# Kernel tuning notes

Hardware: AMD Instinct MI355X
Metric: run time of the kernel (lower is better)

## Reference

```python
import jax, jax.numpy as jnp
import numpy as np

D_MODEL = 512
BINS = 64


def setup_inputs() -> dict:
    key = jax.random.key(0)
    ks = jax.random.split(key, 5)
    x = jax.random.normal(ks[0], (1, 512, D_MODEL), dtype=jnp.float32)
    # torch Linear(2d, d): weight [d, 2d]; store transposed [2d, d] for x @ W
    s1 = 1.0 / np.sqrt(2 * D_MODEL)
    W1 = jax.random.uniform(ks[1], (2 * D_MODEL, D_MODEL), jnp.float32, -s1, s1)
    b1 = jax.random.uniform(ks[2], (D_MODEL,), jnp.float32, -s1, s1)
    s2 = 1.0 / np.sqrt(D_MODEL)
    W2 = jax.random.uniform(ks[3], (D_MODEL, BINS), jnp.float32, -s2, s2)
    b2 = jax.random.uniform(ks[4], (BINS,), jnp.float32, -s2, s2)
    return {"x": x, "W1": W1, "b1": b1, "W2": W2, "b2": b2}


def reference(x, W1, b1, W2, b2):
    # pair = cat([xi, xj], -1); Linear(cat) == xi @ W1[:d] + xj @ W1[d:]
    # This factorization is exact and avoids materializing the [B,N,N,2d] tensor.
    d = x.shape[-1]
    hi = jnp.einsum('bnd,de->bne', x, W1[:d])      # [B, N, d]
    hj = jnp.einsum('bnd,de->bne', x, W1[d:])      # [B, N, d]
    h = hi[:, :, None, :] + hj[:, None, :, :] + b1  # [B, N, N, d]
    h = jax.nn.gelu(h, approximate=False)           # torch nn.GELU default is exact
    return jnp.einsum('bijd,de->bije', h, W2) + b2  # [B, N, N, bins]
```

## Files before the change

### kernel.cpp

```cpp
#include <hip/hip_runtime.h>
#include <hip/hip_fp16.h>

#define D 512
#define NTOK 512
#define BINS 64

typedef float v4f __attribute__((ext_vector_type(4)));
typedef int v4i __attribute__((ext_vector_type(4)));
typedef short short8 __attribute__((ext_vector_type(8)));
typedef _Float16 h8 __attribute__((ext_vector_type(8)));
typedef _Float16 h4 __attribute__((ext_vector_type(4)));

__device__ __forceinline__ __half2 gelu2(__half2 x) {
    __half2 a = __builtin_bit_cast(__half2, __builtin_bit_cast(int, x) & 0x7fff7fff);
    __half2 s = __hmul2(a, a);
    __half2 m = __hfma2(s, __float2half2_rn(-0.1029437f),
                           __float2half2_rn(-2.3022082f));
    __half2 q = __hmul2(a, m);
    __half2 e = h2exp2(q);
    __half2 n = __hfma2(e, __float2half2_rn(0.228584f),  __float2half2_rn(-0.675920f));
    n = __hfma2(e, n, __float2half2_rn(0.946902f));
    n = __hfma2(e, n, __float2half2_rn(-0.998521f));
    __half2 p = __hfma2(e, n, __float2half2_rn(1.0f));
    __half2 xneg = __hmul2(__hsub2(x, a), __float2half2_rn(0.5f));
    return __hfma2(a, p, xneg);
}

__device__ __forceinline__ __half2 bc_h2(int v) { return __builtin_bit_cast(__half2, v); }
__device__ __forceinline__ int bc_i(__half2 v) { return __builtin_bit_cast(int, v); }

__device__ __forceinline__ v4i pack8(v4f a, v4f b) {
    h8 o;
    o[0] = (_Float16)a.x; o[1] = (_Float16)a.y; o[2] = (_Float16)a.z; o[3] = (_Float16)a.w;
    o[4] = (_Float16)b.x; o[5] = (_Float16)b.y; o[6] = (_Float16)b.z; o[7] = (_Float16)b.w;
    return __builtin_bit_cast(v4i, o);
}

__global__ __launch_bounds__(256) void k_pack(const float* __restrict__ x,
                                              const float* __restrict__ W1,
                                              const float* __restrict__ W2,
                                              v4i* __restrict__ Ap,
                                              v4i* __restrict__ Wp,
                                              short8* __restrict__ Bp) {
    const int b = blockIdx.x;
    const int t = threadIdx.x;
    if (b < 32) {
        const int rb = b;
#pragma unroll
        for (int u = 0; u < 4; ++u) {
            const int e = t + 256 * u;
            const int l = e & 63, ks = e >> 6;
            const float* src = x + (size_t)(rb * 16 + (l & 15)) * D + ks * 32 + (l >> 4) * 8;
            v4f a = *(const v4f*)src;
            v4f c = *(const v4f*)(src + 4);
            Ap[(size_t)(rb * 16 + ks) * 64 + l] = pack8(a, c);
        }
    } else if (b < 288) {
        const int slot = (b - 32) * 256 + t;
        const int l = slot & 63;
        const int ks = (slot >> 6) & 15;
        const int nb = slot >> 10;
        const int ng = nb * 16 + (l & 15);
        const float* src = W1 + (size_t)((ng >> 9) * D + ks * 32 + (l >> 4) * 8) * D
                              + (ng & 511);
        h8 o;
#pragma unroll
        for (int j = 0; j < 8; ++j) o[j] = (_Float16)src[(size_t)j * D];
        Wp[(size_t)(nb * 16 + ks) * 64 + l] = __builtin_bit_cast(v4i, o);
    } else {
        const int tid = (b - 288) * 256 + t;
        const int ll = tid & 63;
        const int nt = (tid >> 6) & 3;
        const int kt = tid >> 8;
        const int colp = nt * 16 + (ll & 15);
        const int krow = kt * 32 + (ll >> 4) * 8;
        short8 v;
#pragma unroll
        for (int u = 0; u < 8; ++u) {
            _Float16 hv = (_Float16)W2[(size_t)(krow + u) * BINS + colp];
            v[u] = __builtin_bit_cast(short, hv);
        }
        Bp[tid] = v;
    }
}

__global__ __launch_bounds__(256) void k_gemm(const v4i* __restrict__ Ap,
                                              const v4i* __restrict__ Wp,
                                              const float* __restrict__ b1,
                                              _Float16* __restrict__ hi,
                                              _Float16* __restrict__ hj) {
    const int l = threadIdx.x & 63;
    const int w = threadIdx.x >> 6;
    const int c = l & 15;
    const int q = l >> 4;
    const int mb = blockIdx.x >> 4;
    const int cb = blockIdx.x & 15;
    const int nb = cb * 4 + w;

    const v4i* ap = Ap + (size_t)mb * 16 * 64 + l;
    const v4i* wp = Wp + (size_t)nb * 16 * 64 + l;

    v4f acc = {0.f, 0.f, 0.f, 0.f};
#pragma unroll 4
    for (int ks = 0; ks < 16; ++ks) {
        v4i a0 = ap[ks * 64];
        v4i bb = wp[ks * 64];
        acc = __builtin_amdgcn_mfma_f32_16x16x32_f16(__builtin_bit_cast(h8, a0),
                                                     __builtin_bit_cast(h8, bb), acc, 0, 0, 0);
    }

    const int ng = nb * 16 + c;
    const float b1v = (ng < D) ? b1[ng] : 0.0f;
    _Float16* dst = (ng < D ? hi : hj) + (ng & 511);
    const int row0 = mb * 16 + q * 4;
#pragma unroll
    for (int r = 0; r < 4; ++r)
        dst[(size_t)(row0 + r) * D] = (_Float16)(acc[r] + b1v);
}

__global__ __launch_bounds__(256, 4) void k_main(const __half* __restrict__ hi,
                                                 const __half* __restrict__ hj,
                                                 const v4i* __restrict__ Bp,
                                                 const float* __restrict__ b2,
                                                 float* __restrict__ out) {
    const int l = threadIdx.x & 63;
    const int w = threadIdx.x >> 6;
    const int c = l & 15;
    const int q = l >> 4;
    const int ib = (blockIdx.x >> 5) * 16;
    const int j0 = (blockIdx.x & 31) * 16;

    const __half* hjp = hj + (size_t)(j0 + c) * D + q * 8;
    const __half* hip = hi + (size_t)(ib + w * 4) * D + q * 8;
    const v4i* bp = Bp + l;

    v4f acc[4][4] = {};

    for (int kt = 0; kt < 16; ++kt) {
        const int ko = kt * 32;
        v4i hjraw = *(const v4i*)(hjp + ko);
        __half2 j0h = bc_h2(hjraw.x), j1h = bc_h2(hjraw.y);
        __half2 j2h = bc_h2(hjraw.z), j3h = bc_h2(hjraw.w);
        v4i bfr[4];
#pragma unroll
        for (int nt = 0; nt < 4; ++nt)
            bfr[nt] = bp[(kt * 4 + nt) * 64];
#pragma unroll
        for (int p = 0; p < 4; ++p) {
            v4i ar = *(const v4i*)(hip + (size_t)p * D + ko);
            __half2 g0 = gelu2(__hadd2(bc_h2(ar.x), j0h));
            __half2 g1 = gelu2(__hadd2(bc_h2(ar.y), j1h));
            __half2 g2 = gelu2(__hadd2(bc_h2(ar.z), j2h));
            __half2 g3 = gelu2(__hadd2(bc_h2(ar.w), j3h));
            v4i ai = {bc_i(g0), bc_i(g1), bc_i(g2), bc_i(g3)};
            h8 af = __builtin_bit_cast(h8, ai);
#pragma unroll
            for (int nt = 0; nt < 4; ++nt)
                acc[p][nt] = __builtin_amdgcn_mfma_f32_16x16x32_f16(
                    af, __builtin_bit_cast(h8, bfr[nt]), acc[p][nt], 0, 0, 0);
        }
    }

    const int i0 = ib + w * 4;
#pragma unroll
    for (int p = 0; p < 4; ++p) {
        const size_t rowbase = ((size_t)(i0 + p) * NTOK + j0 + q * 4) * BINS;
#pragma unroll
        for (int nt = 0; nt < 4; ++nt) {
            const float bb = b2[nt * 16 + c];
            float* op = out + rowbase + nt * 16 + c;
#pragma unroll
            for (int rr = 0; rr < 4; ++rr)
                op[(size_t)rr * BINS] = acc[p][nt][rr] + bb;
        }
    }
}

extern "C" void kernel_launch(void* const* d_in, const int* in_sizes, int n_in,
                              void* d_out, int out_size, void* d_ws, size_t ws_size,
                              hipStream_t stream) {
    const float* x  = (const float*)d_in[0];
    const float* W1 = (const float*)d_in[1];
    const float* b1 = (const float*)d_in[2];
    const float* W2 = (const float*)d_in[3];
    const float* b2 = (const float*)d_in[4];
    float* out = (float*)d_out;

    char* ws = (char*)d_ws;
    __half* hi = (__half*)ws;
    __half* hj = (__half*)(ws + (512u << 10));
    short8* Bp = (short8*)(ws + (1u << 20));
    v4i*    Ap = (v4i*)(ws + (1u << 20) + (64u << 10));
    v4i*    Wp = (v4i*)(ws + (1u << 20) + (64u << 10) + (512u << 10));

    k_pack<<<304, 256, 0, stream>>>(x, W1, W2, Ap, Wp, Bp);
    k_gemm<<<512, 256, 0, stream>>>(Ap, Wp, b1, (_Float16*)hi, (_Float16*)hj);
    k_main<<<1024, 256, 0, stream>>>(hi, hj, (const v4i*)Bp, b2, out);
}
```

Baseline: 130.5 us.

## Stage k_main operands through multi-buffered LDS with async global-to-LDS loads

The main kernel now stages the W2 fragments, the hj tile and the hi rows for each k-step into a 5-slot LDS ring using global_load_lds, issued three steps ahead. Explicit vmcnt waits and a barrier gate each step. Each block then loads shared operands from global memory once instead of every wave fetching them separately, and the loads overlap with the GELU and MFMA work. In exchange it uses about 30 KB of LDS per block, lowers the occupancy hint from 4 to 3 blocks, and adds a barrier on every iteration.

```diff
diff --git a/kernel.cpp b/kernel.cpp
--- a/kernel.cpp
+++ b/kernel.cpp
@@ -9,7 +9,6 @@
 typedef int v4i __attribute__((ext_vector_type(4)));
 typedef short short8 __attribute__((ext_vector_type(8)));
 typedef _Float16 h8 __attribute__((ext_vector_type(8)));
-typedef _Float16 h4 __attribute__((ext_vector_type(4)));
 
 __device__ __forceinline__ __half2 gelu2(__half2 x) {
     __half2 a = __builtin_bit_cast(__half2, __builtin_bit_cast(int, x) & 0x7fff7fff);
@@ -36,6 +35,15 @@
     return __builtin_bit_cast(v4i, o);
 }
 
+__device__ __forceinline__ void g2lds16(const void* g, void* l) {
+    __builtin_amdgcn_global_load_lds(
+        (const __attribute__((address_space(1))) void*)g,
+        (__attribute__((address_space(3))) void*)l, 16, 0, 0);
+}
+
+#define WAITVM_(N) asm volatile("s_waitcnt vmcnt(" #N ")" ::: "memory")
+#define WAITVM(N) WAITVM_(N)
+
 __global__ __launch_bounds__(256) void k_pack(const float* __restrict__ x,
                                               const float* __restrict__ W1,
                                               const float* __restrict__ W2,
@@ -118,10 +126,12 @@
         dst[(size_t)(row0 + r) * D] = (_Float16)(acc[r] + b1v);
 }
 
-__global__ __launch_bounds__(256, 4) void k_main(const __half* __restrict__ hi,
+#define NBUF 5
+#define BUFSZ 6144
+__global__ __launch_bounds__(256, 3) void k_main(const __half* __restrict__ hi,
                                                  const __half* __restrict__ hj,
-                                                 const v4i* __restrict__ Bp,
                                                  const float* __restrict__ b2,
+                                                 const char* __restrict__ BpB,
                                                  float* __restrict__ out) {
     const int l = threadIdx.x & 63;
     const int w = threadIdx.x >> 6;
@@ -130,24 +140,51 @@
     const int ib = (blockIdx.x >> 5) * 16;
     const int j0 = (blockIdx.x & 31) * 16;
 
-    const __half* hjp = hj + (size_t)(j0 + c) * D + q * 8;
-    const __half* hip = hi + (size_t)(ib + w * 4) * D + q * 8;
-    const v4i* bp = Bp + l;
+    __shared__ __align__(16) char lds[NBUF * BUFSZ];
+
+    const char* hjB = (const char*)hj;
+    const char* hiB = (const char*)hi;
+
+#define STAGE(kt_, bi_)                                                          \
+    {                                                                            \
+        char* buf_ = lds + (bi_) * BUFSZ;                                        \
+        g2lds16(BpB + (size_t)(kt_) * 4096 + (w * 64 + l) * 16, buf_ + w * 1024);\
+        if (w == 0)                                                              \
+            g2lds16(hjB + (size_t)(j0 + (l & 15)) * 1024 + (kt_) * 64 + (l >> 4) * 16, \
+                    buf_ + 4096);                                                \
+        if (w == 1)                                                              \
+            g2lds16(hiB + (size_t)(ib + (l >> 2)) * 1024 + (kt_) * 64 + (l & 3) * 16,  \
+                    buf_ + 5120);                                                \
+    }
 
     v4f acc[4][4] = {};
 
+    STAGE(0, 0) STAGE(1, 1) STAGE(2, 2)
+
+#pragma unroll
     for (int kt = 0; kt < 16; ++kt) {
-        const int ko = kt * 32;
-        v4i hjraw = *(const v4i*)(hjp + ko);
+        if (kt + 3 < 16) STAGE(kt + 3, (kt + 3) % NBUF)
+        const int rem = (kt <= 12) ? 3 : 15 - kt;
+        if (w < 2) {
+            if (rem == 3) WAITVM(6); else if (rem == 2) WAITVM(4);
+            else if (rem == 1) WAITVM(2); else WAITVM(0);
+        } else {
+            if (rem == 3) WAITVM(3); else if (rem == 2) WAITVM(2);
+            else if (rem == 1) WAITVM(1); else WAITVM(0);
+        }
+        __builtin_amdgcn_s_barrier();
+
+        const char* buf = lds + (kt % NBUF) * BUFSZ;
+        const v4i* bsec = (const v4i*)buf;
+        v4i bfr[4];
+#pragma unroll
+        for (int nt = 0; nt < 4; ++nt) bfr[nt] = bsec[nt * 64 + l];
+        v4i hjraw = ((const v4i*)(buf + 4096))[l];
         __half2 j0h = bc_h2(hjraw.x), j1h = bc_h2(hjraw.y);
         __half2 j2h = bc_h2(hjraw.z), j3h = bc_h2(hjraw.w);
-        v4i bfr[4];
-#pragma unroll
-        for (int nt = 0; nt < 4; ++nt)
-            bfr[nt] = bp[(kt * 4 + nt) * 64];
 #pragma unroll
         for (int p = 0; p < 4; ++p) {
-            v4i ar = *(const v4i*)(hip + (size_t)p * D + ko);
+            v4i ar = *(const v4i*)(buf + 5120 + ((w * 4 + p) * 4 + q) * 16);
             __half2 g0 = gelu2(__hadd2(bc_h2(ar.x), j0h));
             __half2 g1 = gelu2(__hadd2(bc_h2(ar.y), j1h));
             __half2 g2 = gelu2(__hadd2(bc_h2(ar.z), j2h));
@@ -160,6 +197,7 @@
                     af, __builtin_bit_cast(h8, bfr[nt]), acc[p][nt], 0, 0, 0);
         }
     }
+#undef STAGE
 
     const int i0 = ib + w * 4;
 #pragma unroll
@@ -195,5 +233,5 @@
 
     k_pack<<<304, 256, 0, stream>>>(x, W1, W2, Ap, Wp, Bp);
     k_gemm<<<512, 256, 0, stream>>>(Ap, Wp, b1, (_Float16*)hi, (_Float16*)hj);
-    k_main<<<1024, 256, 0, stream>>>(hi, hj, (const v4i*)Bp, b2, out);
-}
+    k_main<<<1024, 256, 0, stream>>>(hi, hj, b2, (const char*)Bp, out);
+}
```

After: 125.8 us. 1.04x faster.
